# Optimization experiments

Hardware: AMD Instinct MI355X
Metric: run time of the kernel (lower is better)

## Reference

```python
import jax, jax.numpy as jnp
import numpy as np

D_MODEL = 1024
N_HEAD = 16
D_K = 64
D_V = 64
SEQ = 4096


def setup_inputs() -> dict:
    key = jax.random.key(0)
    ks = jax.random.split(key, 7)
    s = 1.0 / np.sqrt(D_MODEL)
    return {
        "q": jax.random.normal(ks[0], (SEQ, D_MODEL), dtype=jnp.float32),
        "k": jax.random.normal(ks[1], (SEQ, D_MODEL), dtype=jnp.float32),
        "v": jax.random.normal(ks[2], (SEQ, D_MODEL), dtype=jnp.float32),
        "Wq": jax.random.normal(ks[3], (N_HEAD * D_K, D_MODEL), dtype=jnp.float32) * s,
        "Wk": jax.random.normal(ks[4], (N_HEAD * D_K, D_MODEL), dtype=jnp.float32) * s,
        "Wv": jax.random.normal(ks[5], (N_HEAD * D_V, D_MODEL), dtype=jnp.float32) * s,
        "Wfc": jax.random.normal(ks[6], (D_MODEL, N_HEAD * D_V), dtype=jnp.float32) * s,
    }


def reference(q, k, v, Wq, Wk, Wv, Wfc):
    len_q = q.shape[0]
    residual = q
    temperature = jnp.asarray(np.sqrt(D_K), q.dtype)
    # projections: [len, n_head, d_k] -> [n_head, len, d_k]
    qh = (q @ Wq.T).reshape(len_q, N_HEAD, D_K).transpose(1, 0, 2)
    kh = (k @ Wk.T).reshape(k.shape[0], N_HEAD, D_K).transpose(1, 0, 2)
    vh = (v @ Wv.T).reshape(v.shape[0], N_HEAD, D_V).transpose(1, 0, 2)
    # scores: [n_head, len_q, len_k]
    attn = jnp.einsum('hqd,hkd->hqk', qh / temperature, kh)
    attn = jax.nn.softmax(attn, axis=-1)  # dropout = identity (eval)
    out = jnp.einsum('hqk,hkd->hqd', attn, vh)  # [n_head, len_q, d_v]
    out = out.transpose(1, 0, 2).reshape(len_q, N_HEAD * D_V)
    out = out @ Wfc.T  # dropout = identity (eval)
    return jax.nn.relu(out) + residual
```

## Files before the change

kernel.cpp:

```cpp
#include <hip/hip_runtime.h>
#include <math.h>

#define SEQ    4096
#define DMODEL 1024
#define NHEAD  16
#define DHEAD  64
#define KVHALF 2048

typedef __bf16 bf16;
typedef bf16  bf16x4 __attribute__((ext_vector_type(4)));
typedef bf16  bf16x8 __attribute__((ext_vector_type(8)));
typedef float f32x4  __attribute__((ext_vector_type(4)));
typedef float f32x16 __attribute__((ext_vector_type(16)));
typedef unsigned int u32;

#define SWZ(r)  ((((r) >> 2) ^ (r)) & 7)
#define SWZ3(r) (((r) ^ ((r) >> 2) ^ ((r) >> 3)) & 7)

#define SCQ 0.18033688f

__device__ __forceinline__ void gll16(const void* g, void* l) {
    __builtin_amdgcn_global_load_lds(
        (const __attribute__((address_space(1))) void*)g,
        (__attribute__((address_space(3))) void*)l, 16, 0, 0);
}

__device__ __forceinline__ u32 cvtpk(float lo, float hi) {
    u32 r;
    asm("v_cvt_pk_bf16_f32 %0, %1, %2" : "=v"(r) : "v"(lo), "v"(hi));
    return r;
}
__device__ __forceinline__ void pswap(u32& a, u32& b) {
    asm volatile("v_permlane32_swap_b32 %0, %1" : "+v"(a), "+v"(b));
}

__global__ __launch_bounds__(256)
void cvt_all(const float* __restrict__ q, const float* __restrict__ k,
             const float* __restrict__ v, const float* __restrict__ Wq,
             const float* __restrict__ Wk, const float* __restrict__ Wv,
             const float* __restrict__ Wfc,
             bf16* __restrict__ qb, bf16* __restrict__ kb, bf16* __restrict__ vb,
             bf16* __restrict__ Wqb, bf16* __restrict__ Wkb, bf16* __restrict__ Wvb,
             bf16* __restrict__ Wfcb)
{
    const int b = blockIdx.x;
    const float* s; bf16* d; int base;
    if      (b < 2048) { s = q;   d = qb;   base = b; }
    else if (b < 4096) { s = k;   d = kb;   base = b - 2048; }
    else if (b < 6144) { s = v;   d = vb;   base = b - 4096; }
    else if (b < 6656) { s = Wq;  d = Wqb;  base = b - 6144; }
    else if (b < 7168) { s = Wk;  d = Wkb;  base = b - 6656; }
    else if (b < 7680) { s = Wv;  d = Wvb;  base = b - 7168; }
    else               { s = Wfc; d = Wfcb; base = b - 7680; }
    const int i = (base * 256 + threadIdx.x) * 8;
    float4 a0 = *(const float4*)&s[i];
    float4 a1 = *(const float4*)&s[i + 4];
    bf16x8 o;
    o[0] = (bf16)a0.x; o[1] = (bf16)a0.y; o[2] = (bf16)a0.z; o[3] = (bf16)a0.w;
    o[4] = (bf16)a1.x; o[5] = (bf16)a1.y; o[6] = (bf16)a1.z; o[7] = (bf16)a1.w;
    *(bf16x8*)&d[i] = o;
}

template<int EPI>
__device__ __forceinline__ void gemm_body(
    const bf16* __restrict__ A, const bf16* __restrict__ B,
    bf16* __restrict__ Cb, float* __restrict__ Cf, const float* __restrict__ res,
    int bm, int bn, int N, float scale)
{
    constexpr int K = DMODEL;
    const int tid  = threadIdx.x;
    const int w    = tid >> 6;
    const int lane = tid & 63;
    const int lr   = lane & 15;
    const int lh   = lane >> 4;
    const int wr   = w >> 1;
    const int wc   = w & 1;
    const int lrow = lane >> 3;
    const int lch  = lane & 7;

    __shared__ bf16 As[64 * 64];
    __shared__ bf16 Bs[64 * 64];

    f32x4 acc[2][2] = {};

    for (int k0 = 0; k0 < K; k0 += 64) {
        __syncthreads();
        #pragma unroll
        for (int i = 0; i < 2; ++i) {
            const int r = (w * 2 + i) * 8 + lrow;
            gll16(A + (size_t)(bm + r) * K + k0 + ((lch ^ SWZ(r)) << 3),
                  &As[(w * 2 + i) * 512]);
        }
        #pragma unroll
        for (int i = 0; i < 2; ++i) {
            const int r = (w * 2 + i) * 8 + lrow;
            gll16(B + (size_t)(bn + r) * K + k0 + ((lch ^ SWZ(r)) << 3),
                  &Bs[(w * 2 + i) * 512]);
        }
        asm volatile("s_waitcnt vmcnt(0)" ::: "memory");
        __syncthreads();

        bf16x8 af[2][2], bfr[2][2];
        #pragma unroll
        for (int rt = 0; rt < 2; ++rt)
            #pragma unroll
            for (int s = 0; s < 2; ++s) {
                const int r = wr * 32 + rt * 16 + lr;
                af[rt][s] = *(const bf16x8*)&As[r * 64 + (((s * 4 + lh) ^ SWZ(r)) << 3)];
            }
        #pragma unroll
        for (int ct = 0; ct < 2; ++ct)
            #pragma unroll
            for (int s = 0; s < 2; ++s) {
                const int r = wc * 32 + ct * 16 + lr;
                bfr[ct][s] = *(const bf16x8*)&Bs[r * 64 + (((s * 4 + lh) ^ SWZ(r)) << 3)];
            }
        __builtin_amdgcn_s_setprio(1);
        #pragma unroll
        for (int rt = 0; rt < 2; ++rt)
            #pragma unroll
            for (int ct = 0; ct < 2; ++ct)
                #pragma unroll
                for (int s = 0; s < 2; ++s)
                    acc[rt][ct] = __builtin_amdgcn_mfma_f32_16x16x32_bf16(
                        af[rt][s], bfr[ct][s], acc[rt][ct], 0, 0, 0);
        __builtin_amdgcn_s_setprio(0);
    }

    #pragma unroll
    for (int rt = 0; rt < 2; ++rt)
        #pragma unroll
        for (int ct = 0; ct < 2; ++ct)
            #pragma unroll
            for (int r = 0; r < 4; ++r) {
                const int m = bm + wr * 32 + rt * 16 + lh * 4 + r;
                const int n = bn + wc * 32 + ct * 16 + lr;
                const float vv = acc[rt][ct][r] * scale;
                if (EPI == 0) {
                    Cb[(size_t)m * N + n] = (bf16)vv;
                } else if (EPI == 2) {
                    Cb[(((size_t)(m >> 6) * (size_t)(N >> 6) + (size_t)(n >> 6)) << 12)
                       + ((m & 63) << 6) + (n & 63)] = (bf16)vv;
                } else {
                    Cf[(size_t)m * N + n] =
                        fmaxf(vv, 0.f) + res[(size_t)m * N + n];
                }
            }
}

__global__ __launch_bounds__(256)
void gemm_qkv(const bf16* __restrict__ qb, const bf16* __restrict__ kb,
              const bf16* __restrict__ vb, const bf16* __restrict__ Wqb,
              const bf16* __restrict__ Wkb, const bf16* __restrict__ Wvb,
              bf16* __restrict__ Pq, bf16* __restrict__ Pk, bf16* __restrict__ Pvt)
{
    if (blockIdx.z == 0)
        gemm_body<0>(qb, Wqb, Pq, nullptr, nullptr,
                     blockIdx.y * 64, blockIdx.x * 64, DMODEL, SCQ);
    else if (blockIdx.z == 1)
        gemm_body<0>(kb, Wkb, Pk, nullptr, nullptr,
                     blockIdx.y * 64, blockIdx.x * 64, DMODEL, 1.0f);
    else
        gemm_body<2>(Wvb, vb, Pvt, nullptr, nullptr,
                     blockIdx.x * 64, blockIdx.y * 64, SEQ, 1.0f);
}

__global__ __launch_bounds__(256)
void gemm_fc(const bf16* __restrict__ AO, const bf16* __restrict__ Wfcb,
             float* __restrict__ out, const float* __restrict__ res)
{
    gemm_body<1>(AO, Wfcb, nullptr, out, res,
                 blockIdx.y * 64, blockIdx.x * 64, DMODEL, 1.0f);
}

__global__ __launch_bounds__(256, 4)
void attn_mfma(const bf16* __restrict__ Q, const bf16* __restrict__ K,
               const bf16* __restrict__ Vt_g,
               bf16* __restrict__ Oa, bf16* __restrict__ Ob,
               float* __restrict__ La, float* __restrict__ Lb)
{
    const int wg   = blockIdx.x;
    const int lgc  = (wg & 7) * 128 + (wg >> 3);
    const int half = lgc >> 9;
    const int h    = (lgc >> 5) & 15;
    const int q0   = (lgc & 31) * 128;
    const int c0   = half * KVHALF;

    bf16*  Op = half ? Ob : Oa;
    float* Lp = half ? Lb : La;

    const int tid  = threadIdx.x;
    const int w    = tid >> 6;
    const int lane = tid & 63;
    const int lo5  = lane & 31;
    const int hi   = lane >> 5;
    const int lrow = lane >> 3;
    const int lch  = lane & 7;

    __shared__ bf16 Ks[2][64 * 64];
    __shared__ bf16 Vt[2][64 * 64];

    const bf16* qrow = Q + (size_t)(q0 + w * 32 + lo5) * DMODEL + h * 64;
    bf16x8 qf[4];
    #pragma unroll
    for (int s = 0; s < 4; ++s)
        qf[s] = *(const bf16x8*)&qrow[s * 16 + hi * 8];

    f32x16 acc0 = {}, acc1 = {};
    float lsum = 0.f;

    const int vd  = tid >> 2;
    const int vc2 = (tid & 3) * 2;
    const int voff = vd * 64 + vc2 * 8;
    const int vw0 = vd * 64 + (((vc2 + 0) ^ SWZ3(vd)) << 3);
    const int vw1 = vd * 64 + (((vc2 + 1) ^ SWZ3(vd)) << 3);
    const bf16* Vth = Vt_g + ((size_t)h * (SEQ / 64) << 12);

    #pragma unroll
    for (int i = 0; i < 2; ++i) {
        const int r = (w * 2 + i) * 8 + lrow;
        gll16(K + (size_t)(c0 + r) * DMODEL + h * 64 + ((lch ^ SWZ3(r)) << 3),
              &Ks[0][(w * 2 + i) * 512]);
    }
    {
        const bf16* vt = Vth + (((size_t)(c0 >> 6)) << 12);
        bf16x8 u0 = *(const bf16x8*)&vt[voff];
        bf16x8 u1 = *(const bf16x8*)&vt[voff + 8];
        asm volatile("s_waitcnt vmcnt(0)" ::: "memory");
        *(bf16x8*)&Vt[0][vw0] = u0;
        *(bf16x8*)&Vt[0][vw1] = u1;
    }
    __syncthreads();

#define BODY(CUR, CN)                                                          \
    {                                                                          \
        const int cn = c0 + (((CN) - c0) & (KVHALF - 1));                      \
        _Pragma("unroll")                                                      \
        for (int i = 0; i < 2; ++i) {                                          \
            const int r = (w * 2 + i) * 8 + lrow;                              \
            gll16(K + (size_t)(cn + r) * DMODEL + h * 64 + ((lch ^ SWZ3(r)) << 3), \
                  &Ks[(CUR) ^ 1][(w * 2 + i) * 512]);                          \
        }                                                                      \
        const bf16* vt = Vth + (((size_t)(cn >> 6)) << 12);                    \
        bf16x8 u0 = *(const bf16x8*)&vt[voff];                                 \
        bf16x8 u1 = *(const bf16x8*)&vt[voff + 8];                             \
        const bf16* Kc = Ks[CUR];                                              \
        const bf16* Vc = Vt[CUR];                                              \
        _Pragma("unroll")                                                      \
        for (int kh = 0; kh < 2; ++kh) {                                       \
            const int rr = kh * 32 + lo5;                                      \
            f32x16 st = {};                                                    \
            __builtin_amdgcn_s_setprio(1);                                     \
            _Pragma("unroll")                                                  \
            for (int s = 0; s < 4; ++s) {                                      \
                bf16x8 kf = *(const bf16x8*)&Kc[rr * 64 + (((s * 2 + hi) ^ SWZ3(rr)) << 3)]; \
                st = __builtin_amdgcn_mfma_f32_32x32x16_bf16(kf, qf[s], st, 0, 0, 0); \
            }                                                                  \
            __builtin_amdgcn_s_setprio(0);                                     \
            _Pragma("unroll")                                                  \
            for (int r = 0; r < 16; ++r)                                       \
                st[r] = __builtin_amdgcn_exp2f(fminf(st[r], 50.f));            \
            lsum += (((st[0] + st[1]) + (st[2] + st[3]))                       \
                   + ((st[4] + st[5]) + (st[6] + st[7])))                      \
                  + (((st[8] + st[9]) + (st[10] + st[11]))                     \
                   + ((st[12] + st[13]) + (st[14] + st[15])));                 \
            _Pragma("unroll")                                                  \
            for (int kk = 0; kk < 2; ++kk) {                                   \
                const int ks = kh * 2 + kk;                                    \
                const int b = kk * 8;                                          \
                u32 A0 = cvtpk(st[b + 0], st[b + 1]);                          \
                u32 C0 = cvtpk(st[b + 2], st[b + 3]);                          \
                u32 B0 = cvtpk(st[b + 4], st[b + 5]);                          \
                u32 D0 = cvtpk(st[b + 6], st[b + 7]);                          \
                pswap(A0, B0);                                                 \
                pswap(C0, D0);                                                 \
                union { u32 wd[4]; bf16x8 v; } fr;                             \
                fr.wd[0] = A0; fr.wd[1] = C0; fr.wd[2] = B0; fr.wd[3] = D0;    \
                bf16x8 vf0 = *(const bf16x8*)&Vc[lo5 * 64 + (((ks * 2 + hi) ^ SWZ3(lo5)) << 3)]; \
                bf16x8 vf1 = *(const bf16x8*)&Vc[(32 + lo5) * 64 + (((ks * 2 + hi) ^ SWZ3(32 + lo5)) << 3)]; \
                __builtin_amdgcn_s_setprio(1);                                 \
                acc0 = __builtin_amdgcn_mfma_f32_32x32x16_bf16(vf0, fr.v, acc0, 0, 0, 0); \
                acc1 = __builtin_amdgcn_mfma_f32_32x32x16_bf16(vf1, fr.v, acc1, 0, 0, 0); \
                __builtin_amdgcn_s_setprio(0);                                 \
            }                                                                  \
        }                                                                      \
        asm volatile("s_waitcnt vmcnt(0)" ::: "memory");                       \
        {                                                                      \
            bf16* Vn = Vt[(CUR) ^ 1];                                          \
            *(bf16x8*)&Vn[vw0] = u0;                                           \
            *(bf16x8*)&Vn[vw1] = u1;                                           \
        }                                                                      \
        __syncthreads();                                                       \
    }

    for (int c = c0; c < c0 + KVHALF; c += 128) {
        BODY(0, c + 64)
        BODY(1, c + 128)
    }
#undef BODY

    float lt = lsum;
    lt += __shfl_xor(lt, 32);
    Lp[h * SEQ + q0 + w * 32 + lo5] = lt;

    bf16* orow = Op + (size_t)(q0 + w * 32 + lo5) * DMODEL + h * 64;
    #pragma unroll
    for (int g = 0; g < 4; ++g) {
        bf16x4 o4;
        o4[0] = (bf16)acc0[g * 4 + 0];
        o4[1] = (bf16)acc0[g * 4 + 1];
        o4[2] = (bf16)acc0[g * 4 + 2];
        o4[3] = (bf16)acc0[g * 4 + 3];
        *(bf16x4*)&orow[g * 8 + 4 * hi] = o4;
        bf16x4 o5;
        o5[0] = (bf16)acc1[g * 4 + 0];
        o5[1] = (bf16)acc1[g * 4 + 1];
        o5[2] = (bf16)acc1[g * 4 + 2];
        o5[3] = (bf16)acc1[g * 4 + 3];
        *(bf16x4*)&orow[32 + g * 8 + 4 * hi] = o5;
    }
}

__global__ __launch_bounds__(256)
void combine(const bf16* __restrict__ Oa, const bf16* __restrict__ Ob,
             const float* __restrict__ La, const float* __restrict__ Lb,
             bf16* __restrict__ AO)
{
    const int e   = (blockIdx.x * 256 + threadIdx.x) * 8;
    const int row = e >> 10;
    const int hh  = (e >> 6) & 15;
    const float inv = 1.0f / (La[hh * SEQ + row] + Lb[hh * SEQ + row]);
    bf16x8 a = *(const bf16x8*)&Oa[e];
    bf16x8 b = *(const bf16x8*)&Ob[e];
    bf16x8 o;
    #pragma unroll
    for (int i = 0; i < 8; ++i)
        o[i] = (bf16)(((float)a[i] + (float)b[i]) * inv);
    *(bf16x8*)&AO[e] = o;
}

extern "C" void kernel_launch(void* const* d_in, const int* in_sizes, int n_in,
                              void* d_out, int out_size, void* d_ws, size_t ws_size,
                              hipStream_t stream)
{
    const float* q   = (const float*)d_in[0];
    const float* k   = (const float*)d_in[1];
    const float* v   = (const float*)d_in[2];
    const float* Wq  = (const float*)d_in[3];
    const float* Wk  = (const float*)d_in[4];
    const float* Wv  = (const float*)d_in[5];
    const float* Wfc = (const float*)d_in[6];
    float* out = (float*)d_out;

    const int EM = SEQ * DMODEL;
    const int WM = DMODEL * DMODEL;

    bf16* Wfcb = (bf16*)d_ws;
    bf16* qb   = Wfcb + WM;
    bf16* kb   = qb + EM;
    bf16* vb   = kb + EM;
    bf16* Wqb  = vb + EM;
    bf16* Wkb  = Wqb + WM;
    bf16* Wvb  = Wkb + WM;
    bf16* Pq   = Wvb + WM;
    bf16* Pk   = Pq + EM;
    bf16* Pvt  = Pk + EM;
    bf16* AO   = Pvt + EM;

    bf16*  Oa = qb;
    bf16*  Ob = kb;
    float* La = (float*)vb;
    float* Lb = La + NHEAD * SEQ;

    cvt_all<<<8192, 256, 0, stream>>>(q, k, v, Wq, Wk, Wv, Wfc,
                                      qb, kb, vb, Wqb, Wkb, Wvb, Wfcb);

    gemm_qkv<<<dim3(DMODEL / 64, SEQ / 64, 3), 256, 0, stream>>>(
        qb, kb, vb, Wqb, Wkb, Wvb, Pq, Pk, Pvt);

    attn_mfma<<<1024, 256, 0, stream>>>(Pq, Pk, Pvt, Oa, Ob, La, Lb);

    combine<<<EM / 2048, 256, 0, stream>>>(Oa, Ob, La, Lb, AO);

    gemm_fc<<<dim3(DMODEL / 64, SEQ / 64), 256, 0, stream>>>(AO, Wfcb, out, q);
}
```

Before: 179.7 us.

## Split attention KV range into four chunks instead of two

The attention kernel now splits the key/value sequence into four 1024-long chunks rather than two halves, doubling the grid to 2048 workgroups. Each chunk writes its own partial output and row sums into reused workspace buffers, and the combine kernel reduces four partials instead of two. The goal is more parallelism and better CU fill on a device with many compute units, paid for with extra partial-output traffic in combine and per-block prologue overhead. It also drops the clamp before exp2, which relies on scores staying small enough not to overflow without max subtraction.

New measurement: 178.5 us (median of 2 runs). About the same (-0.7%).

```diff
diff --git a/kernel.cpp b/kernel.cpp
--- a/kernel.cpp
+++ b/kernel.cpp
@@ -5,7 +5,7 @@
 #define DMODEL 1024
 #define NHEAD  16
 #define DHEAD  64
-#define KVHALF 2048
+#define KVQ    1024
 
 typedef __bf16 bf16;
 typedef bf16  bf16x4 __attribute__((ext_vector_type(4)));
@@ -176,18 +176,17 @@
 __global__ __launch_bounds__(256, 4)
 void attn_mfma(const bf16* __restrict__ Q, const bf16* __restrict__ K,
                const bf16* __restrict__ Vt_g,
-               bf16* __restrict__ Oa, bf16* __restrict__ Ob,
-               float* __restrict__ La, float* __restrict__ Lb)
+               bf16* __restrict__ Oabc, bf16* Od, float* __restrict__ Lbase)
 {
     const int wg   = blockIdx.x;
-    const int lgc  = (wg & 7) * 128 + (wg >> 3);
-    const int half = lgc >> 9;
-    const int h    = (lgc >> 5) & 15;
+    const int lgc  = (wg & 7) * 256 + (wg >> 3);
+    const int h    = lgc >> 7;
+    const int qt   = (lgc >> 5) & 3;
     const int q0   = (lgc & 31) * 128;
-    const int c0   = half * KVHALF;
-
-    bf16*  Op = half ? Ob : Oa;
-    float* Lp = half ? Lb : La;
+    const int c0   = qt * KVQ;
+
+    bf16*  Op = (qt < 3) ? (Oabc + (size_t)qt * (SEQ * DMODEL)) : Od;
+    float* Lp = Lbase + qt * (NHEAD * SEQ);
 
     const int tid  = threadIdx.x;
     const int w    = tid >> 6;
@@ -234,7 +233,7 @@
 
 #define BODY(CUR, CN)                                                          \
     {                                                                          \
-        const int cn = c0 + (((CN) - c0) & (KVHALF - 1));                      \
+        const int cn = c0 + (((CN) - c0) & (KVQ - 1));                         \
         _Pragma("unroll")                                                      \
         for (int i = 0; i < 2; ++i) {                                          \
             const int r = (w * 2 + i) * 8 + lrow;                              \
@@ -259,7 +258,7 @@
             __builtin_amdgcn_s_setprio(0);                                     \
             _Pragma("unroll")                                                  \
             for (int r = 0; r < 16; ++r)                                       \
-                st[r] = __builtin_amdgcn_exp2f(fminf(st[r], 50.f));            \
+                st[r] = __builtin_amdgcn_exp2f(st[r]);                         \
             lsum += (((st[0] + st[1]) + (st[2] + st[3]))                       \
                    + ((st[4] + st[5]) + (st[6] + st[7])))                      \
                   + (((st[8] + st[9]) + (st[10] + st[11]))                     \
@@ -293,7 +292,7 @@
         __syncthreads();                                                       \
     }
 
-    for (int c = c0; c < c0 + KVHALF; c += 128) {
+    for (int c = c0; c < c0 + KVQ; c += 128) {
         BODY(0, c + 64)
         BODY(1, c + 128)
     }
@@ -322,20 +321,25 @@
 }
 
 __global__ __launch_bounds__(256)
-void combine(const bf16* __restrict__ Oa, const bf16* __restrict__ Ob,
-             const float* __restrict__ La, const float* __restrict__ Lb,
-             bf16* __restrict__ AO)
-{
+void combine(const bf16* __restrict__ Oabc, const bf16* Od,
+             const float* __restrict__ Lbase, bf16* AO)
+{
+    const int EM  = SEQ * DMODEL;
     const int e   = (blockIdx.x * 256 + threadIdx.x) * 8;
     const int row = e >> 10;
     const int hh  = (e >> 6) & 15;
-    const float inv = 1.0f / (La[hh * SEQ + row] + Lb[hh * SEQ + row]);
-    bf16x8 a = *(const bf16x8*)&Oa[e];
-    bf16x8 b = *(const bf16x8*)&Ob[e];
+    const int li  = hh * SEQ + row;
+    const int HS  = NHEAD * SEQ;
+    const float inv = 1.0f / (Lbase[li] + Lbase[HS + li]
+                            + Lbase[2 * HS + li] + Lbase[3 * HS + li]);
+    bf16x8 a = *(const bf16x8*)&Oabc[e];
+    bf16x8 b = *(const bf16x8*)&Oabc[EM + e];
+    bf16x8 c = *(const bf16x8*)&Oabc[2 * (size_t)EM + e];
+    bf16x8 d = *(const bf16x8*)&Od[e];
     bf16x8 o;
     #pragma unroll
     for (int i = 0; i < 8; ++i)
-        o[i] = (bf16)(((float)a[i] + (float)b[i]) * inv);
+        o[i] = (bf16)((((float)a[i] + (float)b[i]) + ((float)c[i] + (float)d[i])) * inv);
     *(bf16x8*)&AO[e] = o;
 }
 
@@ -367,10 +371,9 @@
     bf16* Pvt  = Pk + EM;
     bf16* AO   = Pvt + EM;
 
-    bf16*  Oa = qb;
-    bf16*  Ob = kb;
-    float* La = (float*)vb;
-    float* Lb = La + NHEAD * SEQ;
+    bf16*  Oabc = qb;
+    bf16*  Od   = AO;
+    float* Lbase = (float*)Wqb;
 
     cvt_all<<<8192, 256, 0, stream>>>(q, k, v, Wq, Wk, Wv, Wfc,
                                       qb, kb, vb, Wqb, Wkb, Wvb, Wfcb);
@@ -378,9 +381,9 @@
     gemm_qkv<<<dim3(DMODEL / 64, SEQ / 64, 3), 256, 0, stream>>>(
         qb, kb, vb, Wqb, Wkb, Wvb, Pq, Pk, Pvt);
 
-    attn_mfma<<<1024, 256, 0, stream>>>(Pq, Pk, Pvt, Oa, Ob, La, Lb);
-
-    combine<<<EM / 2048, 256, 0, stream>>>(Oa, Ob, La, Lb, AO);
+    attn_mfma<<<2048, 256, 0, stream>>>(Pq, Pk, Pvt, Oabc, Od, Lbase);
+
+    combine<<<EM / 2048, 256, 0, stream>>>(Oabc, Od, Lbase, AO);
 
     gemm_fc<<<dim3(DMODEL / 64, SEQ / 64), 256, 0, stream>>>(AO, Wfcb, out, q);
 }
```
